# Optimization experiments

Hardware: AMD Instinct MI355X
Metric: run time of the kernel (lower is better)

The kernel has to match this reference:

```python
import jax, jax.numpy as jnp
import numpy as np

N_CHANNELS = 32
DIM_CAPSULE = 16


def setup_inputs() -> dict:
    key = jax.random.key(0)
    k1, k2, k3 = jax.random.split(key, 3)
    B, H, W, Cin = 32, 56, 56, 256
    d, n = DIM_CAPSULE, N_CHANNELS
    inputs = jax.random.normal(k1, (B, H, W, Cin), dtype=jnp.float32)
    # glorot-ish scale for the 3x3 conv kernel
    convW_1 = jax.random.normal(k2, (3, 3, Cin, d * n), dtype=jnp.float32) * 0.02
    bias_1 = jnp.zeros((d * n,), dtype=jnp.float32)
    CapsAct_W = jax.random.normal(k3, (1, 1, d, d * n), dtype=jnp.float32) * 0.1
    CapsAct_B = jnp.zeros((d * n,), dtype=jnp.float32)
    return {"inputs": inputs, "convW_1": convW_1, "bias_1": bias_1,
            "CapsAct_W": CapsAct_W, "CapsAct_B": CapsAct_B}


def reference(inputs, convW_1, bias_1, CapsAct_W, CapsAct_B):
    d, n = DIM_CAPSULE, N_CHANNELS
    # 3x3 stride-2 SAME conv (NHWC / HWIO), bias, relu
    y = jax.lax.conv_general_dilated(
        inputs, convW_1, window_strides=(2, 2), padding="SAME",
        dimension_numbers=("NHWC", "HWIO", "NHWC"))
    y = jax.nn.relu(y + bias_1)                      # [B, Ho, Wo, d*n]
    B, Ho, Wo, _ = y.shape
    # Per-channel 1x1 convs == grouped matmul over capsule channels.
    yg = y.reshape(B, Ho, Wo, n, d)                  # group channels: [B,Ho,Wo,n,d_in]
    Wg = CapsAct_W.reshape(d, n, d)                  # [d_in, n, d_out]
    bg = CapsAct_B.reshape(n, d)                     # [n, d_out]
    # output layout matches tf: [B, Ho, Wo, dim_capsule, n_channels]
    out = jnp.einsum("bhwnd,dne->bhwen", yg, Wg) + bg.T[None, None, None]
    return out
```

## Files before the change

kernel.cpp:

```cpp
#include <hip/hip_runtime.h>
#include <hip/hip_bf16.h>

typedef __attribute__((ext_vector_type(4))) float f32x4;
typedef __attribute__((ext_vector_type(8))) short s16x8;
typedef __attribute__((ext_vector_type(8))) unsigned short u16x8;
typedef __attribute__((ext_vector_type(4))) unsigned short u16x4;

__device__ __forceinline__ unsigned short bfbits(float f) {
  unsigned int u = __builtin_bit_cast(unsigned int, f);
  return (unsigned short)((u + 0x8000u) >> 16);
}

__device__ __forceinline__ void gll16(void* lds, const void* g) {
  __builtin_amdgcn_global_load_lds(
      (const __attribute__((address_space(1))) unsigned int*)g,
      (__attribute__((address_space(3))) unsigned int*)lds, 16, 0, 0);
}

__global__ __launch_bounds__(256)
void prep_all(const float* __restrict__ in, __hip_bfloat16* __restrict__ dst,
              const float* __restrict__ w, __hip_bfloat16* __restrict__ wt) {
  int t = threadIdx.x;
  if (blockIdx.x < 1824) {
    __shared__ __align__(16) unsigned short row[14848];
    int bh = blockIdx.x;
    int h = bh % 57, b = bh / 57;
    __hip_bfloat16* d = (__hip_bfloat16*)dst + (long)bh * 14848;
    if (h < 56) {
      if (t < 64) {
        int par = t >> 5, cq = t & 31;
        u16x4 z = {0, 0, 0, 0};
        *(u16x4*)(row + (par * 32 + cq) * 232 + 224) = z;
        *(u16x4*)(row + (par * 32 + cq) * 232 + 228) = z;
      }
      const float* src = in + (long)(b * 56 + h) * 56 * 256;
#pragma unroll
      for (int j = 0; j < 14; ++j) {
        int idx = j * 256 + t;
        f32x4 v = *(const f32x4*)(src + idx * 4);
        int e0 = idx * 4;
        int ww = e0 >> 8, c = e0 & 255;
        int off = ((ww & 1) * 32 + (c >> 3)) * 232 + (ww >> 1) * 8 + (c & 7);
        u16x4 q = {bfbits(v[0]), bfbits(v[1]), bfbits(v[2]), bfbits(v[3])};
        *(u16x4*)(row + off) = q;
      }
      __syncthreads();
      for (int i = t; i < 1856; i += 256)
        *(u16x8*)(d + i * 8) = *(const u16x8*)(row + i * 8);
    } else {
      u16x8 z = {0, 0, 0, 0, 0, 0, 0, 0};
      for (int i = t; i < 1856; i += 256) *(u16x8*)(d + i * 8) = z;
    }
  } else {
    int u = (blockIdx.x - 1824) * 256 + t;
    int n = u & 511;
    int c8 = (u >> 9) & 31;
    int kpos = u >> 14;
    int tt = kpos * 8 + (c8 >> 2);
    int cq = c8 & 3;
    const float* src = w + ((kpos * 256 + c8 * 8) * 512) + n;
    u16x8 d;
#pragma unroll
    for (int j = 0; j < 8; ++j) d[j] = bfbits(src[j * 512]);
    int nb = n >> 7, nl = n & 127;
    *reinterpret_cast<u16x8*>(wt + ((tt * 4 + nb) * 4096 + cq * 1024 + nl * 8)) = d;
  }
}

__global__ __launch_bounds__(512, 4)
void caps_main_fast(const __hip_bfloat16* __restrict__ inp,
                    const __hip_bfloat16* __restrict__ wt,
                    const float* __restrict__ bias1,
                    const float* __restrict__ capsW,
                    const float* __restrict__ capsB,
                    float* __restrict__ out) {
  __shared__ __align__(16) unsigned char smem[65536];
  __hip_bfloat16* smem_e = (__hip_bfloat16*)smem;

  int bid = (int)blockIdx.x;
  bid = (bid & 7) * 49 + (bid >> 3);
  int mblk = bid >> 2;
  int nb = bid & 3;
  int p0 = mblk * 256;

  int tid = threadIdx.x;
  int lane = tid & 63;
  int wv = tid >> 6;
  int wm = (wv >> 1) * 64;
  int wn = (wv & 1) * 64;
  int col = lane & 15;
  int lq = lane >> 4;

  int mq = wv >> 1;
  int cqa = (wv & 1) * 2;

  int p = p0 + mq * 64 + lane;
  int b = p / 784;
  int rr = p - b * 784;
  int ho = rr / 28;
  int wo = rr - ho * 28;
  int base0 = b * 846336 + 2 * ho * 14848 + wo * 8;

  const __hip_bfloat16* wtb = wt + nb * 4096;

  f32x4 acc[4][4] = {};

  auto stage = [&](int buf, int t) {
    int kp = t >> 3, tc = t & 7;
    int kh = (kp * 11) >> 5;
    int kw = kp - kh * 3;
    __hip_bfloat16* sa = smem_e + buf * 8192;
    const __hip_bfloat16* as =
        inp + base0 + kh * 14848 + (kw & 1) * 7424 + (kw >> 1) * 8 + (tc * 4 + cqa) * 232;
    gll16(sa + cqa * 2048 + mq * 512, as);
    gll16(sa + (cqa + 1) * 2048 + mq * 512, as + 232);
  };

  stage(0, 0);
  stage(1, 1);
  __asm__ volatile("s_waitcnt vmcnt(2)" ::: "memory");
  __builtin_amdgcn_s_barrier();
  __asm__ volatile("" ::: "memory");

  int rd = 0;
  for (int t = 0; t < 72; ++t) {
    const __hip_bfloat16* sa = smem_e + rd * 8192;
    s16x8 af[4];
#pragma unroll
    for (int mf = 0; mf < 4; ++mf)
      af[mf] = *(const s16x8*)(sa + lq * 2048 + (wm + 16 * mf + col) * 8);
    const __hip_bfloat16* bg = wtb + t * 16384 + lq * 1024;
    s16x8 bq[4];
#pragma unroll
    for (int nf = 0; nf < 4; ++nf)
      bq[nf] = *(const s16x8*)(bg + (wn + 16 * nf + col) * 8);
    __builtin_amdgcn_sched_barrier(0);
    if (t + 2 < 72) {
      int st = rd + 2; if (st >= 3) st -= 3;
      stage(st, t + 2);
    }
    __builtin_amdgcn_s_setprio(1);
#pragma unroll
    for (int mf = 0; mf < 4; ++mf)
#pragma unroll
      for (int nf = 0; nf < 4; ++nf)
        acc[mf][nf] = __builtin_amdgcn_mfma_f32_16x16x32_bf16(
            af[mf], bq[nf], acc[mf][nf], 0, 0, 0);
    __builtin_amdgcn_s_setprio(0);
    if (t < 71) {
      if (t < 70) {
        __asm__ volatile("s_waitcnt vmcnt(2)" ::: "memory");
      } else {
        __asm__ volatile("s_waitcnt vmcnt(0)" ::: "memory");
      }
      __builtin_amdgcn_s_barrier();
      __asm__ volatile("" ::: "memory");
    }
    rd = (rd + 1 == 3) ? 0 : rd + 1;
  }

  int gb = nb * 8 + (wv & 1) * 4;
  s16x8 wf[4];
  f32x4 cinit[4];
#pragma unroll
  for (int g = 0; g < 4; ++g) {
    int gg = gb + g;
    s16x8 bw = {0, 0, 0, 0, 0, 0, 0, 0};
    if (lq < 2) {
#pragma unroll
      for (int j = 0; j < 8; ++j)
        bw[j] = (short)bfbits(capsW[(8 * lq + j) * 512 + gg * 16 + col]);
    }
    wf[g] = bw;
    float cb = capsB[gg * 16 + col];
    cinit[g] = f32x4{cb, cb, cb, cb};
  }
  float b1v[4];
  int nBase = nb * 128 + wn;
#pragma unroll
  for (int nf = 0; nf < 4; ++nf) b1v[nf] = bias1[nBase + nf * 16 + col];

  __asm__ volatile("s_waitcnt vmcnt(0) lgkmcnt(0)" ::: "memory");
  __builtin_amdgcn_s_barrier();
  __asm__ volatile("" ::: "memory");

  __hip_bfloat16* yw = smem_e + wv * 4096;
#pragma unroll
  for (int nf = 0; nf < 4; ++nf) {
#pragma unroll
    for (int mf = 0; mf < 4; ++mf) {
      f32x4 a = acc[mf][nf];
#pragma unroll
      for (int r = 0; r < 4; ++r) {
        int pl = mf * 16 + lq * 4 + r;
        int nl = nf * 16 + col;
        float v = a[r] + b1v[nf];
        v = v > 0.f ? v : 0.f;
        int off = (pl * 128 + nl * 2) ^ ((pl & 7) << 4);
        *(unsigned short*)((char*)yw + off) = bfbits(v);
      }
    }
  }

#pragma unroll
  for (int mf = 0; mf < 4; ++mf) {
    int prow = 16 * mf + col;
    f32x4 dd[4];
#pragma unroll
    for (int g = 0; g < 4; ++g) {
      s16x8 afv = {0, 0, 0, 0, 0, 0, 0, 0};
      if (lq < 2) {
        int off = (prow * 128 + g * 32 + lq * 16) ^ ((prow & 7) << 4);
        afv = *(const s16x8*)((char*)yw + off);
      }
      dd[g] = __builtin_amdgcn_mfma_f32_16x16x32_bf16(afv, wf[g], cinit[g], 0, 0, 0);
    }
    long pgl = (long)(p0 + wm) + 16 * mf;
#pragma unroll
    for (int r = 0; r < 4; ++r) {
      long pg = pgl + 4 * lq + r;
      f32x4 o = {dd[0][r], dd[1][r], dd[2][r], dd[3][r]};
      *(f32x4*)(out + (pg * 16 + col) * 32 + gb) = o;
    }
  }
}

__global__ __launch_bounds__(256, 3)
void caps_main_v1(const float* __restrict__ in, const __hip_bfloat16* __restrict__ wt,
                  const float* __restrict__ bias1, const float* __restrict__ capsW,
                  const float* __restrict__ capsB, float* __restrict__ out) {
  __shared__ __align__(16) unsigned char smem[32768];
  __hip_bfloat16* sA = (__hip_bfloat16*)smem;
  __hip_bfloat16* sB = (__hip_bfloat16*)(smem + 8192);

  int bid = (int)blockIdx.x;
  bid = (bid & 7) * 98 + (bid >> 3);
  int mblk = bid >> 2;
  int nb = bid & 3;
  int p0 = mblk * 128;

  int tid = threadIdx.x;
  int lane = tid & 63;
  int wv = tid >> 6;
  int wm = (wv >> 1) * 64;
  int wn = (wv & 1) * 64;
  int col = lane & 15;
  int lq = lane >> 4;

  int am = tid & 127;
  int ah = tid >> 7;
  int p = p0 + am;
  int bb = p / 784;
  int rr = p - bb * 784;
  int ho = rr / 28;
  int wo = rr - ho * 28;

  f32x4 acc[4][4] = {};
  const __hip_bfloat16* wtb = wt + nb * 4096;

  for (int kp = 0; kp < 9; ++kp) {
    int kh = kp / 3;
    int kw = kp - kh * 3;
    int h = 2 * ho + kh, ww = 2 * wo + kw;
    bool valid = (h < 56) && (ww < 56);
    const float* arow = in + (((bb * 56 + h) * 56 + ww) * 256) + ah * 16;
#pragma unroll
    for (int tc = 0; tc < 8; ++tc) {
      int t = kp * 8 + tc;
      __syncthreads();
      const __hip_bfloat16* bsrc = wtb + t * 16384 + tid * 8;
      gll16(sB + (wv * 512), bsrc);
      gll16(sB + 2048 + (wv * 512), bsrc + 2048);
      f32x4 v0, v1, v2, v3;
      if (valid) {
        const f32x4* apv = (const f32x4*)(arow + tc * 32);
        v0 = apv[0]; v1 = apv[1]; v2 = apv[2]; v3 = apv[3];
      } else {
        v0 = f32x4{0.f, 0.f, 0.f, 0.f}; v1 = v0; v2 = v0; v3 = v0;
      }
      u16x8 pk0, pk1;
#pragma unroll
      for (int j = 0; j < 4; ++j) {
        pk0[j] = bfbits(v0[j]); pk0[j + 4] = bfbits(v1[j]);
        pk1[j] = bfbits(v2[j]); pk1[j + 4] = bfbits(v3[j]);
      }
      *(u16x8*)(sA + (ah * 2) * 1024 + am * 8) = pk0;
      *(u16x8*)(sA + (ah * 2 + 1) * 1024 + am * 8) = pk1;
      __syncthreads();
      s16x8 af[4], bfr[4];
#pragma unroll
      for (int mf = 0; mf < 4; ++mf)
        af[mf] = *(const s16x8*)(sA + lq * 1024 + (wm + 16 * mf + col) * 8);
#pragma unroll
      for (int nf = 0; nf < 4; ++nf)
        bfr[nf] = *(const s16x8*)(sB + lq * 1024 + (wn + 16 * nf + col) * 8);
#pragma unroll
      for (int mf = 0; mf < 4; ++mf)
#pragma unroll
        for (int nf = 0; nf < 4; ++nf)
          acc[mf][nf] = __builtin_amdgcn_mfma_f32_16x16x32_bf16(
              af[mf], bfr[nf], acc[mf][nf], 0, 0, 0);
    }
  }

  __syncthreads();

  __hip_bfloat16* yw = (__hip_bfloat16*)smem + wv * 4096;
  int nBase = nb * 128 + wn;
#pragma unroll
  for (int nf = 0; nf < 4; ++nf) {
    float b1v = bias1[nBase + nf * 16 + col];
#pragma unroll
    for (int mf = 0; mf < 4; ++mf) {
      f32x4 a = acc[mf][nf];
#pragma unroll
      for (int r = 0; r < 4; ++r) {
        int pl = mf * 16 + lq * 4 + r;
        int nl = nf * 16 + col;
        float v = a[r] + b1v;
        v = v > 0.f ? v : 0.f;
        int off = (pl * 128 + nl * 2) ^ ((pl & 7) << 4);
        *(unsigned short*)((char*)yw + off) = bfbits(v);
      }
    }
  }

  int gb = nb * 8 + (wv & 1) * 4;
  s16x8 wf[4];
  f32x4 cinit[4];
#pragma unroll
  for (int g = 0; g < 4; ++g) {
    int gg = gb + g;
    s16x8 bw = {0, 0, 0, 0, 0, 0, 0, 0};
    if (lq < 2) {
#pragma unroll
      for (int j = 0; j < 8; ++j)
        bw[j] = (short)bfbits(capsW[(8 * lq + j) * 512 + gg * 16 + col]);
    }
    wf[g] = bw;
    float cb = capsB[gg * 16 + col];
    cinit[g] = f32x4{cb, cb, cb, cb};
  }
#pragma unroll
  for (int mf = 0; mf < 4; ++mf) {
    int prow = 16 * mf + col;
    f32x4 dd[4];
#pragma unroll
    for (int g = 0; g < 4; ++g) {
      s16x8 afv = {0, 0, 0, 0, 0, 0, 0, 0};
      if (lq < 2) {
        int off = (prow * 128 + g * 32 + lq * 16) ^ ((prow & 7) << 4);
        afv = *(const s16x8*)((char*)yw + off);
      }
      dd[g] = __builtin_amdgcn_mfma_f32_16x16x32_bf16(afv, wf[g], cinit[g], 0, 0, 0);
    }
    long pgl = (long)(p0 + wm) + 16 * mf;
#pragma unroll
    for (int r = 0; r < 4; ++r) {
      long pg = pgl + 4 * lq + r;
      f32x4 o = {dd[0][r], dd[1][r], dd[2][r], dd[3][r]};
      *(f32x4*)(out + (pg * 16 + col) * 32 + gb) = o;
    }
  }
}

extern "C" void kernel_launch(void* const* d_in, const int* in_sizes, int n_in,
                              void* d_out, int out_size, void* d_ws, size_t ws_size,
                              hipStream_t stream) {
  const float* inputs = (const float*)d_in[0];
  const float* convW  = (const float*)d_in[1];
  const float* bias1  = (const float*)d_in[2];
  const float* capsW  = (const float*)d_in[3];
  const float* capsB  = (const float*)d_in[4];
  float* out = (float*)d_out;

  __hip_bfloat16* wt = (__hip_bfloat16*)d_ws;
  const size_t IN_OFF = 2621440;
  const size_t NEED = IN_OFF + (size_t)27082752 * 2;

  if (ws_size >= NEED) {
    __hip_bfloat16* inp = (__hip_bfloat16*)((char*)d_ws + IN_OFF);
    prep_all<<<2400, 256, 0, stream>>>(inputs, inp, convW, wt);
    caps_main_fast<<<392, 512, 0, stream>>>(inp, wt, bias1, capsW, capsB, out);
  } else {
    prep_all<<<2400, 256, 0, stream>>>(inputs, (__hip_bfloat16*)d_ws, convW, wt);
    caps_main_v1<<<784, 256, 0, stream>>>(inputs, wt, bias1, capsW, capsB, out);
  }
}
```

Before: 114.8 us.

## Use 4 waves with 128x64 warp tiles and stage B weights via LDS

The main conv GEMM kernel drops from 8 waves to 4 waves per block. Each wave now computes a 128x64 output tile with 8x4 MFMA accumulators, so every A fragment is reused across more B fragments. The weight tile B is now copied into LDS with direct global-to-LDS loads in the triple-buffered pipeline, where before each wave read it straight from global memory. The LDS footprint grows to 72KB, and the higher register pressure and fewer waves per block may reduce latency hiding.

```diff
diff --git a/kernel.cpp b/kernel.cpp
--- a/kernel.cpp
+++ b/kernel.cpp
@@ -67,14 +67,14 @@
   }
 }
 
-__global__ __launch_bounds__(512, 4)
+__global__ __launch_bounds__(256, 2)
 void caps_main_fast(const __hip_bfloat16* __restrict__ inp,
                     const __hip_bfloat16* __restrict__ wt,
                     const float* __restrict__ bias1,
                     const float* __restrict__ capsW,
                     const float* __restrict__ capsB,
                     float* __restrict__ out) {
-  __shared__ __align__(16) unsigned char smem[65536];
+  __shared__ __align__(16) unsigned char smem[73728];
   __hip_bfloat16* smem_e = (__hip_bfloat16*)smem;
 
   int bid = (int)blockIdx.x;
@@ -86,76 +86,77 @@
   int tid = threadIdx.x;
   int lane = tid & 63;
   int wv = tid >> 6;
-  int wm = (wv >> 1) * 64;
+  int wm2 = (wv >> 1) * 128;
   int wn = (wv & 1) * 64;
   int col = lane & 15;
   int lq = lane >> 4;
 
-  int mq = wv >> 1;
-  int cqa = (wv & 1) * 2;
-
-  int p = p0 + mq * 64 + lane;
-  int b = p / 784;
-  int rr = p - b * 784;
-  int ho = rr / 28;
-  int wo = rr - ho * 28;
-  int base0 = b * 846336 + 2 * ho * 14848 + wo * 8;
+  int baseA[4];
+#pragma unroll
+  for (int pb = 0; pb < 4; ++pb) {
+    int p = p0 + pb * 64 + lane;
+    int b = p / 784;
+    int rr = p - b * 784;
+    int ho = rr / 28;
+    int wo = rr - ho * 28;
+    baseA[pb] = b * 846336 + 2 * ho * 14848 + wo * 8;
+  }
 
   const __hip_bfloat16* wtb = wt + nb * 4096;
 
-  f32x4 acc[4][4] = {};
+  f32x4 acc[8][4] = {};
 
   auto stage = [&](int buf, int t) {
     int kp = t >> 3, tc = t & 7;
     int kh = (kp * 11) >> 5;
     int kw = kp - kh * 3;
-    __hip_bfloat16* sa = smem_e + buf * 8192;
-    const __hip_bfloat16* as =
-        inp + base0 + kh * 14848 + (kw & 1) * 7424 + (kw >> 1) * 8 + (tc * 4 + cqa) * 232;
-    gll16(sa + cqa * 2048 + mq * 512, as);
-    gll16(sa + (cqa + 1) * 2048 + mq * 512, as + 232);
+    int koff = kh * 14848 + (kw & 1) * 7424 + (kw >> 1) * 8 + (tc * 4 + wv) * 232;
+    __hip_bfloat16* sa = smem_e + buf * 12288;
+#pragma unroll
+    for (int pb = 0; pb < 4; ++pb)
+      gll16(sa + wv * 2048 + pb * 512, inp + baseA[pb] + koff);
+    __hip_bfloat16* sb = sa + 8192;
+    const __hip_bfloat16* bs = wtb + t * 16384 + wv * 1024 + lane * 8;
+    gll16(sb + wv * 1024, bs);
+    gll16(sb + wv * 1024 + 512, bs + 512);
   };
 
   stage(0, 0);
   stage(1, 1);
-  __asm__ volatile("s_waitcnt vmcnt(2)" ::: "memory");
+  __asm__ volatile("s_waitcnt vmcnt(6)" ::: "memory");
   __builtin_amdgcn_s_barrier();
   __asm__ volatile("" ::: "memory");
 
   int rd = 0;
   for (int t = 0; t < 72; ++t) {
-    const __hip_bfloat16* sa = smem_e + rd * 8192;
-    s16x8 af[4];
-#pragma unroll
-    for (int mf = 0; mf < 4; ++mf)
-      af[mf] = *(const s16x8*)(sa + lq * 2048 + (wm + 16 * mf + col) * 8);
-    const __hip_bfloat16* bg = wtb + t * 16384 + lq * 1024;
-    s16x8 bq[4];
+    const __hip_bfloat16* sa = smem_e + rd * 12288;
+    const __hip_bfloat16* sb = sa + 8192;
+    s16x8 af[8], bq[4];
+#pragma unroll
+    for (int mf = 0; mf < 8; ++mf)
+      af[mf] = *(const s16x8*)(sa + lq * 2048 + (wm2 + 16 * mf + col) * 8);
 #pragma unroll
     for (int nf = 0; nf < 4; ++nf)
-      bq[nf] = *(const s16x8*)(bg + (wn + 16 * nf + col) * 8);
-    __builtin_amdgcn_sched_barrier(0);
+      bq[nf] = *(const s16x8*)(sb + lq * 1024 + (wn + 16 * nf + col) * 8);
     if (t + 2 < 72) {
       int st = rd + 2; if (st >= 3) st -= 3;
       stage(st, t + 2);
     }
     __builtin_amdgcn_s_setprio(1);
 #pragma unroll
-    for (int mf = 0; mf < 4; ++mf)
+    for (int mf = 0; mf < 8; ++mf)
 #pragma unroll
       for (int nf = 0; nf < 4; ++nf)
         acc[mf][nf] = __builtin_amdgcn_mfma_f32_16x16x32_bf16(
             af[mf], bq[nf], acc[mf][nf], 0, 0, 0);
     __builtin_amdgcn_s_setprio(0);
-    if (t < 71) {
-      if (t < 70) {
-        __asm__ volatile("s_waitcnt vmcnt(2)" ::: "memory");
-      } else {
-        __asm__ volatile("s_waitcnt vmcnt(0)" ::: "memory");
-      }
-      __builtin_amdgcn_s_barrier();
-      __asm__ volatile("" ::: "memory");
-    }
+    if (t < 70) {
+      __asm__ volatile("s_waitcnt vmcnt(6)" ::: "memory");
+    } else if (t == 70) {
+      __asm__ volatile("s_waitcnt vmcnt(0)" ::: "memory");
+    }
+    __builtin_amdgcn_s_barrier();
+    __asm__ volatile("" ::: "memory");
     rd = (rd + 1 == 3) ? 0 : rd + 1;
   }
 
@@ -184,11 +185,11 @@
   __builtin_amdgcn_s_barrier();
   __asm__ volatile("" ::: "memory");
 
-  __hip_bfloat16* yw = smem_e + wv * 4096;
+  __hip_bfloat16* yw = smem_e + wv * 8192;
 #pragma unroll
   for (int nf = 0; nf < 4; ++nf) {
 #pragma unroll
-    for (int mf = 0; mf < 4; ++mf) {
+    for (int mf = 0; mf < 8; ++mf) {
       f32x4 a = acc[mf][nf];
 #pragma unroll
       for (int r = 0; r < 4; ++r) {
@@ -201,9 +202,10 @@
       }
     }
   }
-
-#pragma unroll
-  for (int mf = 0; mf < 4; ++mf) {
+  __asm__ volatile("s_waitcnt lgkmcnt(0)" ::: "memory");
+
+#pragma unroll
+  for (int mf = 0; mf < 8; ++mf) {
     int prow = 16 * mf + col;
     f32x4 dd[4];
 #pragma unroll
@@ -215,7 +217,7 @@
       }
       dd[g] = __builtin_amdgcn_mfma_f32_16x16x32_bf16(afv, wf[g], cinit[g], 0, 0, 0);
     }
-    long pgl = (long)(p0 + wm) + 16 * mf;
+    long pgl = (long)(p0 + wm2) + 16 * mf;
 #pragma unroll
     for (int r = 0; r < 4; ++r) {
       long pg = pgl + 4 * lq + r;
@@ -381,7 +383,7 @@
   if (ws_size >= NEED) {
     __hip_bfloat16* inp = (__hip_bfloat16*)((char*)d_ws + IN_OFF);
     prep_all<<<2400, 256, 0, stream>>>(inputs, inp, convW, wt);
-    caps_main_fast<<<392, 512, 0, stream>>>(inp, wt, bias1, capsW, capsB, out);
+    caps_main_fast<<<392, 256, 0, stream>>>(inp, wt, bias1, capsW, capsB, out);
   } else {
     prep_all<<<2400, 256, 0, stream>>>(inputs, (__hip_bfloat16*)d_ws, convW, wt);
     caps_main_v1<<<784, 256, 0, stream>>>(inputs, wt, bias1, capsW, capsB, out);
```

After: 99.17 us, median of 2. 13.6% less time.
